# Performance work log

Hardware: AMD Instinct MI355X
Metric: run time of the kernel (lower is better)

Reference implementation:

```python
import jax, jax.numpy as jnp
import numpy as np

N = 8192   # nodes
M = 8192   # hyperedges
B = 32     # batch
S = 12     # input_dim (time steps / features)
D = 12     # out_dim
H = 8      # heads
NNZ = 262144  # nonzeros in hg (avg degree 32)
ALPHA = 0.2   # leaky relu slope
NEG = -1000000000.0


def _leaky(x):
    return jax.nn.leaky_relu(x, ALPHA)


def setup_inputs() -> dict:
    rng = np.random.default_rng(0)
    flat = np.sort(rng.choice(N * M, size=NNZ, replace=False))
    idx0 = (flat // M).astype(np.int32)  # node index of each incidence
    idx1 = (flat % M).astype(np.int32)   # hyperedge index
    hg = np.zeros((N, M), np.float32)
    hg[idx0, idx1] = 1.0

    key = jax.random.key(0)
    ks = jax.random.split(key, 9)
    sc = 0.3  # xavier-ish scale for 12-dim fan
    return {
        "x": jax.random.normal(ks[0], (B, S, N), jnp.float32),
        "hg": jnp.asarray(hg),
        "idx0": jnp.asarray(idx0),
        "idx1": jnp.asarray(idx1),
        "P": jax.random.normal(ks[1], (S, D), jnp.float32) * sc,
        "W0": jax.random.normal(ks[2], (H, S, D), jnp.float32) * sc,
        "A": jax.random.normal(ks[3], (H, 2 * D), jnp.float32) * sc,
        "W2": jax.random.normal(ks[4], (H, D, D), jnp.float32) * sc,
        "lin_w": jax.random.normal(ks[5], (1, H), jnp.float32) * sc,
        "lin_b": jax.random.normal(ks[6], (1,), jnp.float32) * 0.01,
        "gcn_w": jax.random.normal(ks[7], (D, D), jnp.float32) * sc,
        "gcn_b": jax.random.normal(ks[8], (D,), jnp.float32) * 0.01,
    }


def reference(x, hg, idx0, idx1, P, W0, A, W2, lin_w, lin_b, gcn_w, gcn_b):
    xp = jnp.transpose(x, (0, 2, 1))                    # [B, N, S]
    xP = jnp.einsum('bns,sd->bnd', xp, P)               # [B, N, D]
    e = _leaky(jnp.einsum('nm,bnd->bmd', hg, xP))       # hg.T @ xP -> [B, M, D]

    # Per-head edge attention; torch code only uses batch index 0.
    x0 = xp[0]                                          # [N, S]
    e0 = e[0]                                           # [M, D]
    x_h = jnp.einsum('ns,hsd->hnd', x0, W0)             # [H, N, D]
    e_h = jnp.einsum('md,hdk->hmk', e0, W2)             # [H, M, D]
    a1, a2 = A[:, :D], A[:, D:]                         # split a = [a1 | a2]
    ax = jnp.einsum('hnd,hd->hn', x_h, a1)              # [H, N]
    ae = jnp.einsum('hmd,hd->hm', e_h, a2)              # [H, M]
    atts = _leaky(ax[:, idx0] + ae[:, idx1])            # [H, NNZ]

    # linear over heads: [NNZ, H] @ w.T + b
    mt = jnp.einsum('hz,h->z', atts, lin_w[0]) + lin_b[0]  # [NNZ]

    mask = jnp.where(hg == 0, NEG, 0.0).astype(x.dtype)
    dense = jnp.zeros((N, M), x.dtype).at[idx0, idx1].set(mt) + mask
    att = jax.nn.softmax(dense, axis=1)                 # [N, M]

    occ = jnp.einsum('nm,bmd->bnd', att, e)             # [B, N, D]
    y = _leaky(occ @ gcn_w.T + gcn_b)                   # dropout p=0 -> identity
    return y
```

## Files before the change

kernel.cpp:

```cpp
#include <hip/hip_runtime.h>

namespace {

constexpr int N    = 8192;
constexpr int M    = 8192;
constexpr int B    = 32;
constexpr int S    = 12;
constexpr int D    = 12;
constexpr int H    = 8;
constexpr int NNZ  = 262144;
constexpr float ALPHA = 0.2f;
constexpr int BD   = B * D;
constexpr int BD2  = BD / 2;
constexpr int RU4  = BD / 8;
constexpr int CSC_CAP = 128;
constexpr int CPB  = 8;

__device__ __forceinline__ float leaky(float v) { return v >= 0.0f ? v : ALPHA * v; }

__device__ __forceinline__ float blo(unsigned v) { return __uint_as_float(v << 16); }
__device__ __forceinline__ float bhi(unsigned v) { return __uint_as_float(v & 0xffff0000u); }
__device__ __forceinline__ unsigned bpack(float a, float b) {
  unsigned x = __float_as_uint(a), y = __float_as_uint(b);
  x = (x + 0x7fffu + ((x >> 16) & 1u)) >> 16;
  y = (y + 0x7fffu + ((y >> 16) & 1u)) & 0xffff0000u;
  return x | y;
}

__global__ void k_prep(const float* __restrict__ x, const float* __restrict__ P,
                       const float* __restrict__ W0, const float* __restrict__ A,
                       const int* __restrict__ idx0, unsigned* __restrict__ xPt_u,
                       float* __restrict__ ax, int* __restrict__ row_ptr,
                       int* __restrict__ colfill) {
  __shared__ float w0a_s[H * S];
  int t = blockIdx.x * blockDim.x + threadIdx.x;
  if (blockIdx.x < 32 && threadIdx.x < H * S) {
    int h = threadIdx.x / S;
    float a = 0.f;
#pragma unroll
    for (int d = 0; d < D; ++d) a += W0[threadIdx.x * D + d] * A[h * 2 * D + d];
    w0a_s[threadIdx.x] = a;
  }
  if (t < M) colfill[t] = 0;
  if (t <= N) {
    int lo = 0, hi = NNZ;
    while (lo < hi) {
      int mid = (lo + hi) >> 1;
      if (idx0[mid] < t) lo = mid + 1; else hi = mid;
    }
    row_ptr[t] = lo;
  }
  if (blockIdx.x < 32) __syncthreads();
  if (t >= B * N) return;
  int b = t >> 13, n = t & (N - 1);
  float xv[S];
#pragma unroll
  for (int s = 0; s < S; ++s) xv[s] = x[((size_t)b * S + s) * N + n];
  float a[D];
#pragma unroll
  for (int d = 0; d < D; ++d) {
    float acc = 0.f;
#pragma unroll
    for (int s = 0; s < S; ++s) acc += xv[s] * P[s * D + d];
    a[d] = acc;
  }
#pragma unroll
  for (int i = 0; i < D / 2; ++i)
    xPt_u[(size_t)n * BD2 + b * (D / 2) + i] = bpack(a[2 * i], a[2 * i + 1]);
  if (b == 0) {
#pragma unroll
    for (int h = 0; h < H; ++h) {
      float acc = 0.f;
#pragma unroll
      for (int s = 0; s < S; ++s) acc += xv[s] * w0a_s[h * S + s];
      ax[n * H + h] = acc;
    }
  }
}

__global__ void k_fill_csc(const int* __restrict__ idx0, const int* __restrict__ idx1,
                           int* __restrict__ colfill, int* __restrict__ csc_rows) {
  int z = blockIdx.x * blockDim.x + threadIdx.x;
  if (z >= NNZ) return;
  int c = idx1[z];
  int p = atomicAdd(&colfill[c], 1);
  if (p < CSC_CAP) csc_rows[c * CSC_CAP + p] = idx0[z];
}

__global__ void k_e(const uint4* __restrict__ xPt4, const int* __restrict__ colfill,
                    const int* __restrict__ csc_rows, const float* __restrict__ W2,
                    const float* __restrict__ A, uint4* __restrict__ e4,
                    float* __restrict__ ae) {
  int tid = threadIdx.x;
  int col = tid / RU4, lt = tid - col * RU4;
  int m = blockIdx.x * CPB + col;
  __shared__ int rows[CPB][CSC_CAP];
  __shared__ float w2a_s[H * D];
  __shared__ float e0_s[CPB][D];
  int cnt = min(colfill[m], CSC_CAP);
  for (int j = lt; j < cnt; j += RU4) rows[col][j] = csc_rows[m * CSC_CAP + j];
  if (tid < H * D) {
    int h = tid / D;
    float a = 0.f;
#pragma unroll
    for (int k = 0; k < D; ++k) a += W2[tid * D + k] * A[h * 2 * D + D + k];
    w2a_s[tid] = a;
  }
  __syncthreads();
  float a[8] = {0.f, 0.f, 0.f, 0.f, 0.f, 0.f, 0.f, 0.f};
  for (int j = 0; j < cnt; ++j) {
    uint4 v = xPt4[(size_t)rows[col][j] * RU4 + lt];
    a[0] += blo(v.x); a[1] += bhi(v.x);
    a[2] += blo(v.y); a[3] += bhi(v.y);
    a[4] += blo(v.z); a[5] += bhi(v.z);
    a[6] += blo(v.w); a[7] += bhi(v.w);
  }
#pragma unroll
  for (int k = 0; k < 8; ++k) a[k] = leaky(a[k]);
  uint4 o;
  o.x = bpack(a[0], a[1]); o.y = bpack(a[2], a[3]);
  o.z = bpack(a[4], a[5]); o.w = bpack(a[6], a[7]);
  e4[(size_t)m * RU4 + lt] = o;
  if (lt == 0) {
#pragma unroll
    for (int k = 0; k < 8; ++k) e0_s[col][k] = a[k];
  } else if (lt == 1) {
#pragma unroll
    for (int k = 0; k < 4; ++k) e0_s[col][8 + k] = a[k];
  }
  __syncthreads();
  if (tid < CPB * H) {
    int c = tid / H, h = tid - c * H;
    float s = 0.f;
#pragma unroll
    for (int d = 0; d < D; ++d) s += e0_s[c][d] * w2a_s[h * D + d];
    ae[(blockIdx.x * CPB + c) * H + h] = s;
  }
}

__global__ void k_yw(const int* __restrict__ idx1, const int* __restrict__ row_ptr,
                     const float* __restrict__ ax, const float* __restrict__ ae,
                     const float* __restrict__ lin_w, const float* __restrict__ lin_b,
                     const uint4* __restrict__ e4, const float* __restrict__ gcn_w,
                     const float* __restrict__ gcn_b, float* __restrict__ y) {
  int tid = threadIdx.x;
  int col = tid / RU4, lt = tid - col * RU4;
  int n0 = blockIdx.x * CPB;
  __shared__ float gw_s[D * D];
  __shared__ float gb_s[D];
  __shared__ float ax_s[CPB][H];
  __shared__ float lw_s[H];
  __shared__ float lb_s;
  __shared__ int   beg_s[CPB];
  __shared__ int   cnt_s[CPB];
  __shared__ int   idx_s[CPB][CSC_CAP];
  __shared__ float mt_s[CPB][CSC_CAP];
  __shared__ float occ_s[CPB][BD];

  if (tid < D * D) gw_s[tid] = gcn_w[tid];
  if (tid >= 144 && tid < 144 + D) gb_s[tid - 144] = gcn_b[tid - 144];
  if (tid >= 192 && tid < 192 + CPB * H) {
    int u = tid - 192, r = u >> 3, h = u & 7;
    ax_s[r][h] = ax[(n0 + r) * H + h];
  }
  if (tid >= 256 && tid < 256 + H) lw_s[tid - 256] = lin_w[tid - 256];
  if (tid == 256 + H) lb_s = lin_b[0];
  if (tid < CPB) {
    int b = row_ptr[n0 + tid];
    beg_s[tid] = b;
    cnt_s[tid] = min(row_ptr[n0 + tid + 1] - b, CSC_CAP);
  }
  __syncthreads();
  for (int j = lt; j < cnt_s[col]; j += RU4) idx_s[col][j] = idx1[beg_s[col] + j];
  __syncthreads();
  for (int j0 = tid; j0 < CPB * CSC_CAP; j0 += 384) {
    int r = j0 >> 7, jj = j0 & (CSC_CAP - 1);
    if (jj < cnt_s[r]) {
      int mm = idx_s[r][jj];
      float mv = lb_s;
#pragma unroll
      for (int h = 0; h < H; ++h) mv += lw_s[h] * leaky(ax_s[r][h] + ae[mm * H + h]);
      mt_s[r][jj] = mv;
    }
  }
  __syncthreads();
  {
    int w = tid >> 6, lane = tid & 63;
    for (int r = w; r < CPB; r += 6) {
      int cnt = cnt_s[r];
      if (cnt <= 0) continue;
      float m0 = (lane < cnt) ? mt_s[r][lane] : -3.0e38f;
      float m1 = (lane + 64 < cnt) ? mt_s[r][lane + 64] : -3.0e38f;
      float mx = fmaxf(m0, m1);
#pragma unroll
      for (int off = 32; off; off >>= 1) mx = fmaxf(mx, __shfl_xor(mx, off));
      float p0 = (lane < cnt) ? expf(m0 - mx) : 0.f;
      float p1 = (lane + 64 < cnt) ? expf(m1 - mx) : 0.f;
      float sum = p0 + p1;
#pragma unroll
      for (int off = 32; off; off >>= 1) sum += __shfl_xor(sum, off);
      float inv = 1.0f / sum;
      if (lane < cnt) mt_s[r][lane] = p0 * inv;
      if (lane + 64 < cnt) mt_s[r][lane + 64] = p1 * inv;
    }
  }
  __syncthreads();
  float a[8] = {0.f, 0.f, 0.f, 0.f, 0.f, 0.f, 0.f, 0.f};
  int cnt = cnt_s[col];
  if (cnt > 0) {
    for (int j = 0; j < cnt; ++j) {
      uint4 v = e4[(size_t)idx_s[col][j] * RU4 + lt];
      float w = mt_s[col][j];
      a[0] += w * blo(v.x); a[1] += w * bhi(v.x);
      a[2] += w * blo(v.y); a[3] += w * bhi(v.y);
      a[4] += w * blo(v.z); a[5] += w * bhi(v.z);
      a[6] += w * blo(v.w); a[7] += w * bhi(v.w);
    }
  } else {
    for (int mm = 0; mm < M; ++mm) {
      uint4 v = e4[(size_t)mm * RU4 + lt];
      a[0] += blo(v.x); a[1] += bhi(v.x);
      a[2] += blo(v.y); a[3] += bhi(v.y);
      a[4] += blo(v.z); a[5] += bhi(v.w);
      a[6] += blo(v.w); a[7] += bhi(v.w);
    }
#pragma unroll
    for (int k = 0; k < 8; ++k) a[k] *= (1.0f / (float)M);
  }
#pragma unroll
  for (int k = 0; k < 8; ++k) occ_s[col][8 * lt + k] = a[k];
  __syncthreads();
  int b = tid / D, d = tid - b * D;
#pragma unroll
  for (int c = 0; c < CPB; ++c) {
    float s = gb_s[d];
#pragma unroll
    for (int k = 0; k < D; ++k) s += occ_s[c][b * D + k] * gw_s[d * D + k];
    y[(size_t)b * N * D + (size_t)(n0 + c) * D + d] = leaky(s);
  }
}

}

extern "C" void kernel_launch(void* const* d_in, const int* in_sizes, int n_in,
                              void* d_out, int out_size, void* d_ws, size_t ws_size,
                              hipStream_t stream) {
  const float* x     = (const float*)d_in[0];
  const int*   idx0  = (const int*)d_in[2];
  const int*   idx1  = (const int*)d_in[3];
  const float* P     = (const float*)d_in[4];
  const float* W0    = (const float*)d_in[5];
  const float* A     = (const float*)d_in[6];
  const float* W2    = (const float*)d_in[7];
  const float* lin_w = (const float*)d_in[8];
  const float* lin_b = (const float*)d_in[9];
  const float* gcn_w = (const float*)d_in[10];
  const float* gcn_b = (const float*)d_in[11];
  float* y = (float*)d_out;

  char* ws = (char*)d_ws;
  size_t off = 0;
  auto carve = [&](size_t bytes) {
    char* p = ws + off;
    off = (off + bytes + 255) & ~(size_t)255;
    return p;
  };
  unsigned* xPt_u   = (unsigned*)carve(sizeof(unsigned) * (size_t)N * BD2);
  unsigned* e_u     = (unsigned*)carve(sizeof(unsigned) * (size_t)M * BD2);
  float*    ax      = (float*)carve(sizeof(float) * N * H);
  float*    ae      = (float*)carve(sizeof(float) * M * H);
  int*      colfill = (int*)carve(sizeof(int) * M);
  int*      row_ptr = (int*)carve(sizeof(int) * (N + 1));
  int*      csc_rows= (int*)carve(sizeof(int) * (size_t)M * CSC_CAP);
  (void)ws_size; (void)in_sizes; (void)n_in; (void)out_size;

  k_prep<<<(B * N + 255) / 256, 256, 0, stream>>>(x, P, W0, A, idx0, xPt_u, ax,
                                                  row_ptr, colfill);
  k_fill_csc<<<(NNZ + 255) / 256, 256, 0, stream>>>(idx0, idx1, colfill, csc_rows);
  k_e<<<M / CPB, 384, 0, stream>>>((const uint4*)xPt_u, colfill, csc_rows, W2, A,
                                   (uint4*)e_u, ae);
  k_yw<<<N / CPB, 384, 0, stream>>>(idx1, row_ptr, ax, ae, lin_w, lin_b,
                                    (const uint4*)e_u, gcn_w, gcn_b, y);
}
```

Measured before the change: 67.52 us.

## Split per-column gather across two thread halves with shared-memory reduction

Halves columns per block (CPB 8→4) and assigns two 48-thread groups to each column/row, each accumulating alternate neighbors, then combines the partial sums through shared memory. This doubles the number of blocks and halves the serial gather-loop length per thread in both the hyperedge aggregation and the attention-weighted node aggregation, which raises memory-level parallelism for the latency-bound gathers. It adds an extra shared buffer and a barrier per block. It also changes the empty-row fallback so that lane a[5] accumulates bhi(v.z) instead of bhi(v.w).

```diff
diff --git a/kernel.cpp b/kernel.cpp
--- a/kernel.cpp
+++ b/kernel.cpp
@@ -14,7 +14,7 @@
 constexpr int BD2  = BD / 2;
 constexpr int RU4  = BD / 8;
 constexpr int CSC_CAP = 128;
-constexpr int CPB  = 8;
+constexpr int CPB  = 4;
 
 __device__ __forceinline__ float leaky(float v) { return v >= 0.0f ? v : ALPHA * v; }
 
@@ -26,6 +26,18 @@
   y = (y + 0x7fffu + ((y >> 16) & 1u)) & 0xffff0000u;
   return x | y;
 }
+
+#define GACC(v)                                        \
+  a[0] += blo((v).x); a[1] += bhi((v).x);              \
+  a[2] += blo((v).y); a[3] += bhi((v).y);              \
+  a[4] += blo((v).z); a[5] += bhi((v).z);              \
+  a[6] += blo((v).w); a[7] += bhi((v).w);
+
+#define WACC(v, wt)                                          \
+  a[0] += (wt) * blo((v).x); a[1] += (wt) * bhi((v).x);      \
+  a[2] += (wt) * blo((v).y); a[3] += (wt) * bhi((v).y);      \
+  a[4] += (wt) * blo((v).z); a[5] += (wt) * bhi((v).z);      \
+  a[6] += (wt) * blo((v).w); a[7] += (wt) * bhi((v).w);
 
 __global__ void k_prep(const float* __restrict__ x, const float* __restrict__ P,
                        const float* __restrict__ W0, const float* __restrict__ A,
@@ -92,13 +104,17 @@
                     const float* __restrict__ A, uint4* __restrict__ e4,
                     float* __restrict__ ae) {
   int tid = threadIdx.x;
-  int col = tid / RU4, lt = tid - col * RU4;
+  int col = tid / 96;
+  int r96 = tid - col * 96;
+  int sub = r96 / 48;
+  int lt  = r96 - sub * 48;
   int m = blockIdx.x * CPB + col;
   __shared__ int rows[CPB][CSC_CAP];
+  __shared__ float part_s[CPB][384];
   __shared__ float w2a_s[H * D];
   __shared__ float e0_s[CPB][D];
   int cnt = min(colfill[m], CSC_CAP);
-  for (int j = lt; j < cnt; j += RU4) rows[col][j] = csc_rows[m * CSC_CAP + j];
+  for (int j = r96; j < cnt; j += 96) rows[col][j] = csc_rows[m * CSC_CAP + j];
   if (tid < H * D) {
     int h = tid / D;
     float a = 0.f;
@@ -108,25 +124,29 @@
   }
   __syncthreads();
   float a[8] = {0.f, 0.f, 0.f, 0.f, 0.f, 0.f, 0.f, 0.f};
-  for (int j = 0; j < cnt; ++j) {
+  for (int j = sub; j < cnt; j += 2) {
     uint4 v = xPt4[(size_t)rows[col][j] * RU4 + lt];
-    a[0] += blo(v.x); a[1] += bhi(v.x);
-    a[2] += blo(v.y); a[3] += bhi(v.y);
-    a[4] += blo(v.z); a[5] += bhi(v.z);
-    a[6] += blo(v.w); a[7] += bhi(v.w);
-  }
-#pragma unroll
-  for (int k = 0; k < 8; ++k) a[k] = leaky(a[k]);
-  uint4 o;
-  o.x = bpack(a[0], a[1]); o.y = bpack(a[2], a[3]);
-  o.z = bpack(a[4], a[5]); o.w = bpack(a[6], a[7]);
-  e4[(size_t)m * RU4 + lt] = o;
-  if (lt == 0) {
-#pragma unroll
-    for (int k = 0; k < 8; ++k) e0_s[col][k] = a[k];
-  } else if (lt == 1) {
-#pragma unroll
-    for (int k = 0; k < 4; ++k) e0_s[col][8 + k] = a[k];
+    GACC(v);
+  }
+  if (sub == 1) {
+#pragma unroll
+    for (int k = 0; k < 8; ++k) part_s[col][lt * 8 + k] = a[k];
+  }
+  __syncthreads();
+  if (sub == 0) {
+#pragma unroll
+    for (int k = 0; k < 8; ++k) a[k] = leaky(a[k] + part_s[col][lt * 8 + k]);
+    uint4 o;
+    o.x = bpack(a[0], a[1]); o.y = bpack(a[2], a[3]);
+    o.z = bpack(a[4], a[5]); o.w = bpack(a[6], a[7]);
+    e4[(size_t)m * RU4 + lt] = o;
+    if (lt == 0) {
+#pragma unroll
+      for (int k = 0; k < 8; ++k) e0_s[col][k] = a[k];
+    } else if (lt == 1) {
+#pragma unroll
+      for (int k = 0; k < 4; ++k) e0_s[col][8 + k] = a[k];
+    }
   }
   __syncthreads();
   if (tid < CPB * H) {
@@ -144,7 +164,10 @@
                      const uint4* __restrict__ e4, const float* __restrict__ gcn_w,
                      const float* __restrict__ gcn_b, float* __restrict__ y) {
   int tid = threadIdx.x;
-  int col = tid / RU4, lt = tid - col * RU4;
+  int col = tid / 96;
+  int r96 = tid - col * 96;
+  int sub = r96 / 48;
+  int lt  = r96 - sub * 48;
   int n0 = blockIdx.x * CPB;
   __shared__ float gw_s[D * D];
   __shared__ float gb_s[D];
@@ -155,23 +178,24 @@
   __shared__ int   cnt_s[CPB];
   __shared__ int   idx_s[CPB][CSC_CAP];
   __shared__ float mt_s[CPB][CSC_CAP];
+  __shared__ float part_s[CPB][384];
   __shared__ float occ_s[CPB][BD];
 
   if (tid < D * D) gw_s[tid] = gcn_w[tid];
   if (tid >= 144 && tid < 144 + D) gb_s[tid - 144] = gcn_b[tid - 144];
-  if (tid >= 192 && tid < 192 + CPB * H) {
-    int u = tid - 192, r = u >> 3, h = u & 7;
+  if (tid >= 160 && tid < 160 + CPB * H) {
+    int u = tid - 160, r = u >> 3, h = u & 7;
     ax_s[r][h] = ax[(n0 + r) * H + h];
   }
-  if (tid >= 256 && tid < 256 + H) lw_s[tid - 256] = lin_w[tid - 256];
-  if (tid == 256 + H) lb_s = lin_b[0];
+  if (tid >= 192 && tid < 192 + H) lw_s[tid - 192] = lin_w[tid - 192];
+  if (tid == 192 + H) lb_s = lin_b[0];
   if (tid < CPB) {
     int b = row_ptr[n0 + tid];
     beg_s[tid] = b;
     cnt_s[tid] = min(row_ptr[n0 + tid + 1] - b, CSC_CAP);
   }
   __syncthreads();
-  for (int j = lt; j < cnt_s[col]; j += RU4) idx_s[col][j] = idx1[beg_s[col] + j];
+  for (int j = r96; j < cnt_s[col]; j += 96) idx_s[col][j] = idx1[beg_s[col] + j];
   __syncthreads();
   for (int j0 = tid; j0 < CPB * CSC_CAP; j0 += 384) {
     int r = j0 >> 7, jj = j0 & (CSC_CAP - 1);
@@ -186,49 +210,54 @@
   __syncthreads();
   {
     int w = tid >> 6, lane = tid & 63;
-    for (int r = w; r < CPB; r += 6) {
+    if (w < CPB) {
+      int r = w;
       int cnt = cnt_s[r];
-      if (cnt <= 0) continue;
-      float m0 = (lane < cnt) ? mt_s[r][lane] : -3.0e38f;
-      float m1 = (lane + 64 < cnt) ? mt_s[r][lane + 64] : -3.0e38f;
-      float mx = fmaxf(m0, m1);
-#pragma unroll
-      for (int off = 32; off; off >>= 1) mx = fmaxf(mx, __shfl_xor(mx, off));
-      float p0 = (lane < cnt) ? expf(m0 - mx) : 0.f;
-      float p1 = (lane + 64 < cnt) ? expf(m1 - mx) : 0.f;
-      float sum = p0 + p1;
-#pragma unroll
-      for (int off = 32; off; off >>= 1) sum += __shfl_xor(sum, off);
-      float inv = 1.0f / sum;
-      if (lane < cnt) mt_s[r][lane] = p0 * inv;
-      if (lane + 64 < cnt) mt_s[r][lane + 64] = p1 * inv;
+      if (cnt > 0) {
+        float m0 = (lane < cnt) ? mt_s[r][lane] : -3.0e38f;
+        float m1 = (lane + 64 < cnt) ? mt_s[r][lane + 64] : -3.0e38f;
+        float mx = fmaxf(m0, m1);
+#pragma unroll
+        for (int off = 32; off; off >>= 1) mx = fmaxf(mx, __shfl_xor(mx, off));
+        float p0 = (lane < cnt) ? expf(m0 - mx) : 0.f;
+        float p1 = (lane + 64 < cnt) ? expf(m1 - mx) : 0.f;
+        float sum = p0 + p1;
+#pragma unroll
+        for (int off = 32; off; off >>= 1) sum += __shfl_xor(sum, off);
+        float inv = 1.0f / sum;
+        if (lane < cnt) mt_s[r][lane] = p0 * inv;
+        if (lane + 64 < cnt) mt_s[r][lane + 64] = p1 * inv;
+      }
     }
   }
   __syncthreads();
   float a[8] = {0.f, 0.f, 0.f, 0.f, 0.f, 0.f, 0.f, 0.f};
   int cnt = cnt_s[col];
   if (cnt > 0) {
-    for (int j = 0; j < cnt; ++j) {
+    for (int j = sub; j < cnt; j += 2) {
       uint4 v = e4[(size_t)idx_s[col][j] * RU4 + lt];
-      float w = mt_s[col][j];
-      a[0] += w * blo(v.x); a[1] += w * bhi(v.x);
-      a[2] += w * blo(v.y); a[3] += w * bhi(v.y);
-      a[4] += w * blo(v.z); a[5] += w * bhi(v.z);
-      a[6] += w * blo(v.w); a[7] += w * bhi(v.w);
+      float wt = mt_s[col][j];
+      WACC(v, wt);
     }
   } else {
-    for (int mm = 0; mm < M; ++mm) {
+    for (int mm = sub; mm < M; mm += 2) {
       uint4 v = e4[(size_t)mm * RU4 + lt];
-      a[0] += blo(v.x); a[1] += bhi(v.x);
-      a[2] += blo(v.y); a[3] += bhi(v.y);
-      a[4] += blo(v.z); a[5] += bhi(v.w);
-      a[6] += blo(v.w); a[7] += bhi(v.w);
-    }
-#pragma unroll
-    for (int k = 0; k < 8; ++k) a[k] *= (1.0f / (float)M);
-  }
-#pragma unroll
-  for (int k = 0; k < 8; ++k) occ_s[col][8 * lt + k] = a[k];
+      GACC(v);
+    }
+  }
+  if (sub == 1) {
+#pragma unroll
+    for (int k = 0; k < 8; ++k) part_s[col][lt * 8 + k] = a[k];
+  }
+  __syncthreads();
+  if (sub == 0) {
+#pragma unroll
+    for (int k = 0; k < 8; ++k) {
+      float v = a[k] + part_s[col][lt * 8 + k];
+      if (cnt <= 0) v *= (1.0f / (float)M);
+      occ_s[col][8 * lt + k] = v;
+    }
+  }
   __syncthreads();
   int b = tid / D, d = tid - b * D;
 #pragma unroll
```

New measurement: 80.44 us. 1.19x slower.
